# Performance work log

Hardware: AMD Instinct MI355X
Metric: run time of the kernel (lower is better)

## Reference

```python
import jax, jax.numpy as jnp
import numpy as np
import math

B, D, C = 2048, 512, 10572


def setup_inputs() -> dict:
    key = jax.random.key(0)
    k1, k2, k3 = jax.random.split(key, 3)
    feat = jax.random.normal(k1, (B, D), dtype=jnp.float32)
    label = jax.random.randint(k2, (B,), 0, C, dtype=jnp.int64)
    # xavier-uniform init for the class weight matrix [C, D]
    limit = math.sqrt(6.0 / (C + D))
    weights = jax.random.uniform(k3, (C, D), dtype=jnp.float32, minval=-limit, maxval=limit)
    return {"feat": feat, "label": label, "weights": weights}


def reference(feat, label, weights):
    class_num = weights.shape[0]
    scale = math.sqrt(2.0) * math.log(class_num - 1)  # auto-scale init, overrides ctor arg
    pi = math.pi

    # L2-normalize features and class weights, cosine similarity logits
    nf = feat / jnp.linalg.norm(feat, axis=-1, keepdims=True)
    nw = weights / jnp.linalg.norm(weights, axis=-1, keepdims=True)
    cos = jnp.matmul(nf, nw.T)          # [B, C]
    logits = scale * cos                 # [B, C]
    probs = jax.nn.softmax(logits, axis=-1)  # detached in original

    idx = jnp.arange(cos.shape[0])
    cos_gt = cos[idx, label]             # [B] cosine at ground-truth class
    logit_gt = logits[idx, label]
    p_gt = probs[idx, label]

    theta = jnp.arccos(cos_gt)           # radians
    thetas_deg = theta / pi * 180.0
    B_vals = jnp.exp(logit_gt) * (1.0 / p_gt - 1.0)

    # clamp angle to < pi/2 before margin rescale
    d_theta = jnp.where(theta >= pi / 2.0, pi / 2.0 - 0.01, theta)
    s = (1.0 / cos_gt) * jnp.log(B_vals * (pi / (2.0 * d_theta) - 1.0))
    s = jax.lax.stop_gradient(s)         # s built from .data/.numpy() (detached) in torch

    # scatter per-sample rescaled logit back at the ground-truth column
    new_logits = logits.at[idx, label].set(s * cos_gt)

    avg_p = jnp.mean(p_gt)
    min_p = jnp.min(p_gt)
    max_p = jnp.max(p_gt)
    B_avg = jnp.arccos(jnp.log(jnp.mean(B_vals) / (class_num - 1)) / scale) / pi * 180.0
    # (thetas stats are printed only in the original; avg kept implicit)
    _ = (jnp.min(thetas_deg), jnp.max(thetas_deg), jnp.mean(thetas_deg))

    return (cos, new_logits, avg_p, min_p, max_p, B_avg, 0, 0)
```

## Files before the change

kernel.cpp:

```cpp
#include <hip/hip_runtime.h>
#include <hip/hip_bf16.h>
#include <cmath>

#define B_ROWS 2048
#define D_DIM 512
#define C_COLS 10572
#define WPAD 10624

#define BM 128
#define BN 128
#define BK 32
#define NSTEP (D_DIM / BK)

typedef __attribute__((ext_vector_type(8))) short short8;
typedef __attribute__((ext_vector_type(4))) float f32x4;

__device__ __host__ inline int swz(int a) { return a ^ (((a >> 7) & 7) << 4); }

__device__ inline void load_lds16(const void* g, const void* l) {
    __builtin_amdgcn_global_load_lds(
        (const __attribute__((address_space(1))) unsigned int*)g,
        (__attribute__((address_space(3))) unsigned int*)l, 16, 0, 0);
}

__global__ __launch_bounds__(256) void normsplit_kernel(const float* __restrict__ x,
                                                        int nrows,
                                                        __hip_bfloat16* __restrict__ hi,
                                                        float* __restrict__ rowsum) {
    int row = blockIdx.x;
    int tid = threadIdx.x;
    size_t base = (size_t)row * D_DIM;
    if (rowsum && tid == 0) rowsum[row] = 0.0f;
    if (row >= nrows) {
        __hip_bfloat16 z = __float2bfloat16(0.0f);
        hi[base + tid] = z;
        hi[base + tid + 256] = z;
        return;
    }
    const float* xr = x + base;
    float a = xr[tid];
    float b = xr[tid + 256];
    float ss = a * a + b * b;
#pragma unroll
    for (int off = 32; off > 0; off >>= 1) ss += __shfl_down(ss, off);
    __shared__ float red[4];
    __shared__ float rbc;
    if ((tid & 63) == 0) red[tid >> 6] = ss;
    __syncthreads();
    if (tid == 0) rbc = 1.0f / sqrtf(red[0] + red[1] + red[2] + red[3]);
    __syncthreads();
    float rn = rbc;
    hi[base + tid] = __float2bfloat16(a * rn);
    hi[base + tid + 256] = __float2bfloat16(b * rn);
}

__global__ __launch_bounds__(256) void gemm_bf16_kernel(
    const __hip_bfloat16* __restrict__ fhi, const __hip_bfloat16* __restrict__ whi,
    float* __restrict__ cosm, float* __restrict__ logits, float* __restrict__ rowsum,
    float scale) {
    __shared__ __hip_bfloat16 Abuf[2][BM * BK];
    __shared__ __hip_bfloat16 Bbuf[2][BN * BK];

    int tid = threadIdx.x;
    int lane = tid & 63;
    int w = tid >> 6;
    int wr = w >> 1, wc = w & 1;

    int orig = blockIdx.y * gridDim.x + blockIdx.x;
    int s = (orig & 7) * 166 + (orig >> 3);
    int by = s & 15;
    int bx = s >> 4;
    int row0 = by * BM;
    int col0 = bx * BN;

    int grow[2], gcol[2], ldsw[2];
#pragma unroll
    for (int i = 0; i < 2; ++i) {
        int o = i * 4096 + tid * 16;
        int q = swz(o);
        grow[i] = q >> 6;
        gcol[i] = (q & 63) >> 1;
        ldsw[i] = i * 4096 + w * 1024;
    }

    int r = lane & 15, kb = lane >> 4;
    int aoff[4], boff[4];
#pragma unroll
    for (int m = 0; m < 4; ++m) {
        aoff[m] = swz((wr * 64 + m * 16 + r) * 64 + kb * 16);
        boff[m] = swz((wc * 64 + m * 16 + r) * 64 + kb * 16);
    }

    const __hip_bfloat16* Ap = fhi + (size_t)row0 * D_DIM;
    const __hip_bfloat16* Bp = whi + (size_t)col0 * D_DIM;

    f32x4 acc[4][4] = {};

#pragma unroll
    for (int i = 0; i < 2; ++i) {
        size_t go = (size_t)grow[i] * D_DIM + gcol[i];
        load_lds16(Ap + go, (const char*)Abuf[0] + ldsw[i]);
        load_lds16(Bp + go, (const char*)Bbuf[0] + ldsw[i]);
    }
    __syncthreads();

    int cur = 0;
    for (int t = 0; t < NSTEP; ++t) {
        if (t < NSTEP - 1) {
            int k0 = (t + 1) * BK;
#pragma unroll
            for (int i = 0; i < 2; ++i) {
                size_t go = (size_t)grow[i] * D_DIM + k0 + gcol[i];
                load_lds16(Ap + go, (const char*)Abuf[cur ^ 1] + ldsw[i]);
                load_lds16(Bp + go, (const char*)Bbuf[cur ^ 1] + ldsw[i]);
            }
        }
        short8 af[4], bf[4];
#pragma unroll
        for (int m = 0; m < 4; ++m)
            af[m] = *(const short8*)((const char*)Abuf[cur] + aoff[m]);
#pragma unroll
        for (int n = 0; n < 4; ++n)
            bf[n] = *(const short8*)((const char*)Bbuf[cur] + boff[n]);
        __builtin_amdgcn_s_setprio(1);
#pragma unroll
        for (int m = 0; m < 4; ++m)
#pragma unroll
            for (int n = 0; n < 4; ++n)
                acc[m][n] = __builtin_amdgcn_mfma_f32_16x16x32_bf16(af[m], bf[n],
                                                                    acc[m][n], 0, 0, 0);
        __builtin_amdgcn_s_setprio(0);
        __syncthreads();
        cur ^= 1;
    }

#pragma unroll
    for (int m = 0; m < 4; ++m) {
#pragma unroll
        for (int j = 0; j < 4; ++j) {
            int rrow = row0 + wr * 64 + m * 16 + (lane >> 4) * 4 + j;
            float se = 0.f;
#pragma unroll
            for (int n = 0; n < 4; ++n) {
                int ccol = col0 + wc * 64 + n * 16 + (lane & 15);
                float v = acc[m][n][j];
                if (ccol < C_COLS) {
                    size_t o = (size_t)rrow * C_COLS + ccol;
                    cosm[o] = v;
                    logits[o] = scale * v;
                    se += __expf(scale * v);
                }
            }
#pragma unroll
            for (int off = 1; off < 16; off <<= 1) se += __shfl_xor(se, off);
            if ((lane & 15) == 0) atomicAdd(&rowsum[rrow], se);
        }
    }
}

__global__ __launch_bounds__(256) void gt_fix_kernel(
    const float* __restrict__ feat, const float* __restrict__ weights,
    const int* __restrict__ label, const float* __restrict__ rowsum,
    float* __restrict__ cosm, float* __restrict__ logits,
    float* __restrict__ pgt, float* __restrict__ bvals, float scale) {
    int row = blockIdx.x * 4 + (threadIdx.x >> 6);
    int lane = threadIdx.x & 63;
    if (row >= B_ROWS) return;
    int lbl = label[row];
    const float4* f4 = (const float4*)(feat + (size_t)row * D_DIM);
    const float4* w4 = (const float4*)(weights + (size_t)lbl * D_DIM);
    float ff = 0.f, ww = 0.f, fw = 0.f;
#pragma unroll
    for (int i = 0; i < 2; ++i) {
        float4 a = f4[lane + i * 64];
        float4 b = w4[lane + i * 64];
        ff += a.x * a.x + a.y * a.y + a.z * a.z + a.w * a.w;
        ww += b.x * b.x + b.y * b.y + b.z * b.z + b.w * b.w;
        fw += a.x * b.x + a.y * b.y + a.z * b.z + a.w * b.w;
    }
#pragma unroll
    for (int off = 32; off > 0; off >>= 1) {
        ff += __shfl_xor(ff, off);
        ww += __shfl_xor(ww, off);
        fw += __shfl_xor(fw, off);
    }
    if (lane == 0) {
        float cg = fw / (sqrtf(ff) * sqrtf(ww));
        float S = rowsum[row];
        float e = expf(scale * cg);
        float p = e / S;
        float Bv = S - e;
        const float PI = 3.14159265358979323846f;
        float marg;
        if (cg > 0.f) {
            marg = asinf(cg) / acosf(cg);
        } else {
            float dth = 0.5f * PI - 0.01f;
            marg = PI / (2.0f * dth) - 1.0f;
        }
        size_t o = (size_t)row * C_COLS + lbl;
        cosm[o] = cg;
        logits[o] = logf(Bv * marg);
        pgt[row] = p;
        bvals[row] = Bv;
    }
}

__global__ __launch_bounds__(256) void finalize_kernel(const float* __restrict__ pgt,
                                                       const float* __restrict__ bvals,
                                                       float* __restrict__ tail,
                                                       float scale) {
    int tid = threadIdx.x;
    float s = 0.f, mn = 1e30f, mx = -1e30f, sb = 0.f;
    for (int i = tid; i < B_ROWS; i += 256) {
        float p = pgt[i];
        s += p;
        mn = fminf(mn, p);
        mx = fmaxf(mx, p);
        sb += bvals[i];
    }
#pragma unroll
    for (int off = 32; off > 0; off >>= 1) {
        s += __shfl_down(s, off);
        mn = fminf(mn, __shfl_down(mn, off));
        mx = fmaxf(mx, __shfl_down(mx, off));
        sb += __shfl_down(sb, off);
    }
    __shared__ float rs[4], rmn[4], rmx[4], rsb[4];
    int wave = tid >> 6;
    if ((tid & 63) == 0) { rs[wave] = s; rmn[wave] = mn; rmx[wave] = mx; rsb[wave] = sb; }
    __syncthreads();
    if (tid == 0) {
        float S = 0.f, MN = 1e30f, MX = -1e30f, SB = 0.f;
        for (int ww = 0; ww < 4; ++ww) {
            S += rs[ww]; MN = fminf(MN, rmn[ww]); MX = fmaxf(MX, rmx[ww]); SB += rsb[ww];
        }
        const float PI = 3.14159265358979323846f;
        tail[0] = S / (float)B_ROWS;
        tail[1] = MN;
        tail[2] = MX;
        float meanB = SB / (float)B_ROWS;
        tail[3] = acosf(logf(meanB / (float)(C_COLS - 1)) / scale) / PI * 180.0f;
        tail[4] = 0.0f;
        tail[5] = 0.0f;
    }
}

extern "C" void kernel_launch(void* const* d_in, const int* in_sizes, int n_in,
                              void* d_out, int out_size, void* d_ws, size_t ws_size,
                              hipStream_t stream) {
    const float* feat = (const float*)d_in[0];
    const int* label = (const int*)d_in[1];
    const float* weights = (const float*)d_in[2];

    float* out = (float*)d_out;
    float* cos_out = out;
    float* logits_out = out + (size_t)B_ROWS * C_COLS;
    float* tail = out + (size_t)2 * B_ROWS * C_COLS;

    double scale_d = std::sqrt(2.0) * std::log((double)(C_COLS - 1));
    float scale = (float)scale_d;

    const size_t fsz = (size_t)B_ROWS * D_DIM * sizeof(__hip_bfloat16);
    const size_t wsz = (size_t)WPAD * D_DIM * sizeof(__hip_bfloat16);
    char* wsb = (char*)d_ws;
    __hip_bfloat16* fhi = (__hip_bfloat16*)wsb;
    __hip_bfloat16* whi = (__hip_bfloat16*)(wsb + fsz);
    float* rowsum = (float*)(wsb + fsz + wsz);
    float* pgt = rowsum + B_ROWS;
    float* bv = pgt + B_ROWS;

    normsplit_kernel<<<B_ROWS, 256, 0, stream>>>(feat, B_ROWS, fhi, rowsum);
    normsplit_kernel<<<WPAD, 256, 0, stream>>>(weights, C_COLS, whi, nullptr);

    dim3 grid(WPAD / BN, B_ROWS / BM);
    gemm_bf16_kernel<<<grid, 256, 0, stream>>>(fhi, whi, cos_out, logits_out, rowsum,
                                               scale);

    gt_fix_kernel<<<B_ROWS / 4, 256, 0, stream>>>(feat, weights, label, rowsum, cos_out,
                                                  logits_out, pgt, bv, scale);
    finalize_kernel<<<1, 256, 0, stream>>>(pgt, bv, tail, scale);
}
```

Measured before the change: 82.52 us.

## Triple-buffer GEMM LDS pipeline and merge normalization into one wave-per-row kernel

The GEMM moves from double- to triple-buffered LDS staging with a prefetch distance of two. It uses explicit vmcnt waits and raw barriers in place of __syncthreads, so global loads overlap the MFMA work over a longer window. The two row-normalization launches become a single kernel that handles one row per wavefront with vectorized loads and stores and no shared-memory reduction. This removes a launch and the block-level syncs, at the cost of more LDS per GEMM block, which may reduce occupancy. It also depends on hand-counted vmcnt values matching the number of loads actually issued.

```diff
diff --git a/kernel.cpp b/kernel.cpp
--- a/kernel.cpp
+++ b/kernel.cpp
@@ -23,43 +23,52 @@
         (__attribute__((address_space(3))) unsigned int*)l, 16, 0, 0);
 }
 
-__global__ __launch_bounds__(256) void normsplit_kernel(const float* __restrict__ x,
-                                                        int nrows,
-                                                        __hip_bfloat16* __restrict__ hi,
-                                                        float* __restrict__ rowsum) {
-    int row = blockIdx.x;
-    int tid = threadIdx.x;
-    size_t base = (size_t)row * D_DIM;
-    if (rowsum && tid == 0) rowsum[row] = 0.0f;
-    if (row >= nrows) {
-        __hip_bfloat16 z = __float2bfloat16(0.0f);
-        hi[base + tid] = z;
-        hi[base + tid + 256] = z;
-        return;
-    }
-    const float* xr = x + base;
-    float a = xr[tid];
-    float b = xr[tid + 256];
-    float ss = a * a + b * b;
-#pragma unroll
-    for (int off = 32; off > 0; off >>= 1) ss += __shfl_down(ss, off);
-    __shared__ float red[4];
-    __shared__ float rbc;
-    if ((tid & 63) == 0) red[tid >> 6] = ss;
-    __syncthreads();
-    if (tid == 0) rbc = 1.0f / sqrtf(red[0] + red[1] + red[2] + red[3]);
-    __syncthreads();
-    float rn = rbc;
-    hi[base + tid] = __float2bfloat16(a * rn);
-    hi[base + tid + 256] = __float2bfloat16(b * rn);
+__global__ __launch_bounds__(256) void normcast_kernel(
+    const float* __restrict__ feat, const float* __restrict__ wts,
+    __hip_bfloat16* __restrict__ fhi, __hip_bfloat16* __restrict__ whi,
+    float* __restrict__ rowsum) {
+    int idx = blockIdx.x * 4 + (threadIdx.x >> 6);
+    int lane = threadIdx.x & 63;
+    const float* src;
+    __hip_bfloat16* dst;
+    if (idx < B_ROWS) {
+        src = feat + (size_t)idx * D_DIM;
+        dst = fhi + (size_t)idx * D_DIM;
+        if (lane == 0) rowsum[idx] = 0.0f;
+    } else {
+        int r = idx - B_ROWS;
+        dst = whi + (size_t)r * D_DIM;
+        if (r >= C_COLS) {
+            short8 z = {0, 0, 0, 0, 0, 0, 0, 0};
+            *(short8*)(dst + lane * 8) = z;
+            return;
+        }
+        src = wts + (size_t)r * D_DIM;
+    }
+    float4 a = *(const float4*)(src + lane * 8);
+    float4 b = *(const float4*)(src + lane * 8 + 4);
+    float ss = a.x * a.x + a.y * a.y + a.z * a.z + a.w * a.w +
+               b.x * b.x + b.y * b.y + b.z * b.z + b.w * b.w;
+#pragma unroll
+    for (int off = 32; off > 0; off >>= 1) ss += __shfl_xor(ss, off);
+    float rn = 1.0f / sqrtf(ss);
+    float v[8] = {a.x * rn, a.y * rn, a.z * rn, a.w * rn,
+                  b.x * rn, b.y * rn, b.z * rn, b.w * rn};
+    short8 o;
+#pragma unroll
+    for (int k = 0; k < 8; ++k) {
+        __hip_bfloat16 h = __float2bfloat16(v[k]);
+        o[k] = *reinterpret_cast<short*>(&h);
+    }
+    *(short8*)(dst + lane * 8) = o;
 }
 
 __global__ __launch_bounds__(256) void gemm_bf16_kernel(
     const __hip_bfloat16* __restrict__ fhi, const __hip_bfloat16* __restrict__ whi,
     float* __restrict__ cosm, float* __restrict__ logits, float* __restrict__ rowsum,
     float scale) {
-    __shared__ __hip_bfloat16 Abuf[2][BM * BK];
-    __shared__ __hip_bfloat16 Bbuf[2][BN * BK];
+    __shared__ __hip_bfloat16 Abuf[3][BM * BK];
+    __shared__ __hip_bfloat16 Bbuf[3][BN * BK];
 
     int tid = threadIdx.x;
     int lane = tid & 63;
@@ -94,34 +103,33 @@
     const __hip_bfloat16* Ap = fhi + (size_t)row0 * D_DIM;
     const __hip_bfloat16* Bp = whi + (size_t)col0 * D_DIM;
 
+    auto stage = [&](int k0, int b) {
+#pragma unroll
+        for (int i = 0; i < 2; ++i) {
+            size_t go = (size_t)grow[i] * D_DIM + k0 + gcol[i];
+            load_lds16(Ap + go, (const char*)&Abuf[b][0] + ldsw[i]);
+            load_lds16(Bp + go, (const char*)&Bbuf[b][0] + ldsw[i]);
+        }
+    };
+
     f32x4 acc[4][4] = {};
 
-#pragma unroll
-    for (int i = 0; i < 2; ++i) {
-        size_t go = (size_t)grow[i] * D_DIM + gcol[i];
-        load_lds16(Ap + go, (const char*)Abuf[0] + ldsw[i]);
-        load_lds16(Bp + go, (const char*)Bbuf[0] + ldsw[i]);
-    }
-    __syncthreads();
-
-    int cur = 0;
+    stage(0, 0);
+    stage(BK, 1);
+    asm volatile("s_waitcnt vmcnt(4)" ::: "memory");
+    __builtin_amdgcn_s_barrier();
+    __builtin_amdgcn_sched_barrier(0);
+
+    int cur = 0, sb = 2;
     for (int t = 0; t < NSTEP; ++t) {
-        if (t < NSTEP - 1) {
-            int k0 = (t + 1) * BK;
-#pragma unroll
-            for (int i = 0; i < 2; ++i) {
-                size_t go = (size_t)grow[i] * D_DIM + k0 + gcol[i];
-                load_lds16(Ap + go, (const char*)Abuf[cur ^ 1] + ldsw[i]);
-                load_lds16(Bp + go, (const char*)Bbuf[cur ^ 1] + ldsw[i]);
-            }
-        }
+        if (t + 2 < NSTEP) stage((t + 2) * BK, sb);
+        const char* Ab = (const char*)&Abuf[cur][0];
+        const char* Bb = (const char*)&Bbuf[cur][0];
         short8 af[4], bf[4];
 #pragma unroll
-        for (int m = 0; m < 4; ++m)
-            af[m] = *(const short8*)((const char*)Abuf[cur] + aoff[m]);
-#pragma unroll
-        for (int n = 0; n < 4; ++n)
-            bf[n] = *(const short8*)((const char*)Bbuf[cur] + boff[n]);
+        for (int m = 0; m < 4; ++m) af[m] = *(const short8*)(Ab + aoff[m]);
+#pragma unroll
+        for (int n = 0; n < 4; ++n) bf[n] = *(const short8*)(Bb + boff[n]);
         __builtin_amdgcn_s_setprio(1);
 #pragma unroll
         for (int m = 0; m < 4; ++m)
@@ -130,8 +138,14 @@
                 acc[m][n] = __builtin_amdgcn_mfma_f32_16x16x32_bf16(af[m], bf[n],
                                                                     acc[m][n], 0, 0, 0);
         __builtin_amdgcn_s_setprio(0);
-        __syncthreads();
-        cur ^= 1;
+        if (t + 2 < NSTEP)
+            asm volatile("s_waitcnt vmcnt(4)" ::: "memory");
+        else
+            asm volatile("s_waitcnt vmcnt(0)" ::: "memory");
+        __builtin_amdgcn_s_barrier();
+        __builtin_amdgcn_sched_barrier(0);
+        cur = (cur == 2) ? 0 : cur + 1;
+        sb = (sb == 2) ? 0 : sb + 1;
     }
 
 #pragma unroll
@@ -270,8 +284,8 @@
     float* pgt = rowsum + B_ROWS;
     float* bv = pgt + B_ROWS;
 
-    normsplit_kernel<<<B_ROWS, 256, 0, stream>>>(feat, B_ROWS, fhi, rowsum);
-    normsplit_kernel<<<WPAD, 256, 0, stream>>>(weights, C_COLS, whi, nullptr);
+    normcast_kernel<<<(B_ROWS + WPAD) / 4, 256, 0, stream>>>(feat, weights, fhi, whi,
+                                                             rowsum);
 
     dim3 grid(WPAD / BN, B_ROWS / BM);
     gemm_bf16_kernel<<<grid, 256, 0, stream>>>(fhi, whi, cos_out, logits_out, rowsum,
```

Result: faster. 75.52 us (-8.5%).
